# Kernel optimization log

Measured on AMD Instinct MI355X. Metric: run time of the kernel, lower is better.

Reference implementation:

```python
import jax, jax.numpy as jnp
import numpy as np

TOKEN_SIZE = 4
NEIGHBOR_SIZE = 3


def setup_inputs() -> dict:
    key = jax.random.key(0)
    ks = jax.random.split(key, 8)
    B, C, H, W = 8, 256, 64, 64
    return {
        "blue_feat": jax.random.normal(ks[0], (B, C, H, W), jnp.float32),
        "white_feat": jax.random.normal(ks[1], (B, C, H, W), jnp.float32),
        "Wq": jax.random.normal(ks[2], (C, C), jnp.float32) * 0.05,
        "bq": jax.random.normal(ks[3], (C,), jnp.float32) * 0.05,
        "Wk": jax.random.normal(ks[4], (C, C), jnp.float32) * 0.05,
        "bk": jax.random.normal(ks[5], (C,), jnp.float32) * 0.05,
        "Wv": jax.random.normal(ks[6], (C, C), jnp.float32) * 0.05,
        "bv": jax.random.normal(ks[7], (C,), jnp.float32) * 0.05,
    }


def _tokens(x, nh, nw, ts):
    # [B,C,H,W] -> [B,nh,nw,C,ts*ts]
    B, C = x.shape[0], x.shape[1]
    return (x.reshape(B, C, nh, ts, nw, ts)
             .transpose(0, 2, 4, 1, 3, 5)
             .reshape(B, nh, nw, C, ts * ts))


def reference(blue_feat, white_feat, Wq, bq, Wk, bk, Wv, bv):
    ts, ns = TOKEN_SIZE, NEIGHBOR_SIZE
    pad = ns // 2
    B, C, H, W = blue_feat.shape
    scale = float((ts * ts) ** -0.5)

    # 1x1 conv projections (pointwise channel mix + bias)
    Q = jnp.einsum('bchw,oc->bohw', blue_feat, Wq) + bq[None, :, None, None]
    K = jnp.einsum('bchw,oc->bohw', white_feat, Wk) + bk[None, :, None, None]
    V = jnp.einsum('bchw,oc->bohw', white_feat, Wv) + bv[None, :, None, None]

    nh, nw = H // ts, W // ts  # H,W divisible by ts -> no padding branch
    Qt = _tokens(Q, nh, nw, ts)  # [B,nh,nw,C,D]
    Kt = _tokens(K, nh, nw, ts)
    Vt = _tokens(V, nh, nw, ts)

    # zero-padded token grid, gather 3x3 neighbor tokens (F.unfold equivalent)
    padw = ((0, 0), (pad, pad), (pad, pad), (0, 0), (0, 0))
    Kp = jnp.pad(Kt, padw)
    Vp = jnp.pad(Vt, padw)
    Knb = jnp.stack([Kp[:, di:di + nh, dj:dj + nw]
                     for di in range(ns) for dj in range(ns)], axis=3)  # [B,nh,nw,9,C,D]
    Vnb = jnp.stack([Vp[:, di:di + nh, dj:dj + nw]
                     for di in range(ns) for dj in range(ns)], axis=3)

    # per-channel attention over neighbor tokens
    attn = jax.nn.softmax(
        jnp.einsum('bhwcd,bhwncd->bhwcn', Qt, Knb) * scale, axis=-1)
    out = jnp.einsum('bhwcn,bhwncd->bhwcd', attn, Vnb)  # [B,nh,nw,C,D]

    enhanced = (out.reshape(B, nh, nw, C, ts, ts)
                   .transpose(0, 3, 1, 4, 2, 5)
                   .reshape(B, C, H, W))
    return blue_feat + enhanced  # out_proj is Identity since c1 == c2
```

## Files before the change

### kernel.cpp

```cpp
#include <hip/hip_runtime.h>
#include <hip/hip_bf16.h>
#include <stdint.h>

typedef float  f32x4  __attribute__((ext_vector_type(4)));
typedef float  f32x2  __attribute__((ext_vector_type(2)));
typedef __bf16 bf16x8 __attribute__((ext_vector_type(8)));

#define LROW 40

__global__ __launch_bounds__(1024) void prep_kernel(
    const float* __restrict__ blue, const float* __restrict__ white,
    const float* __restrict__ Wq, const float* __restrict__ Wk,
    const float* __restrict__ Wv,
    __bf16* __restrict__ Xtb, __bf16* __restrict__ Xtw,
    __bf16* __restrict__ Wbf)
{
  const int bid = blockIdx.x;
  const int tid = threadIdx.x;

  if (bid >= 256) {
    const int t = bid - 256;
    const float* src = (t == 0) ? Wq : (t == 1) ? Wk : Wv;
    __bf16* dst = Wbf + t * 65536;
#pragma unroll
    for (int it = 0; it < 8; ++it) {
      const int idx = it * 8192 + tid * 8;
      f32x4 v0 = *(const f32x4*)(src + idx);
      f32x4 v1 = *(const f32x4*)(src + idx + 4);
      bf16x8 r;
#pragma unroll
      for (int q = 0; q < 4; ++q) { r[q] = (__bf16)v0[q]; r[q + 4] = (__bf16)v1[q]; }
      *(bf16x8*)(dst + idx) = r;
    }
    return;
  }

  const int srcw = bid >> 7;
  const int rem  = bid & 127;
  const int b    = rem >> 4;
  const int ti   = rem & 15;
  const float* X = srcw ? white : blue;
  __bf16*     Xt = srcw ? Xtw : Xtb;

  const int s  = tid & 7;
  const int co = (tid >> 3) & 31;
  const int u  = tid >> 8;

  const float* Xb = X + (size_t)b * (256 * 4096);
  __bf16* Xtb2 = Xt + (size_t)b * 4096 * 256;

#pragma unroll
  for (int it = 0; it < 4; ++it) {
    const int p   = u * 32 + it * 8 + s;
    const int px  = 2 * p;
    const int r   = px >> 6;
    const int col = px & 63;
    const int hw  = (ti * 4 + r) * 64 + col;
    const int d   = r * 4 + (col & 3);
    const int n   = ti * 256 + (col >> 2) * 16 + d;

    bf16x8 e0, e1;
#pragma unroll
    for (int j = 0; j < 8; ++j) {
      const int c = co * 8 + j;
      f32x2 v = *(const f32x2*)(Xb + (size_t)c * 4096 + hw);
      e0[j] = (__bf16)v[0];
      e1[j] = (__bf16)v[1];
    }
    *(bf16x8*)(Xtb2 + (size_t)n * 256 + co * 8)       = e0;
    *(bf16x8*)(Xtb2 + (size_t)(n + 1) * 256 + co * 8) = e1;
  }
}


#define GLOAD16(GS, LD) \
  __builtin_amdgcn_global_load_lds( \
      (const __attribute__((address_space(1))) uint32_t*)(GS), \
      (__attribute__((address_space(3))) uint32_t*)(LD), 16, 0, 0)

__global__ __launch_bounds__(256) void gemm_lds_kernel(
    const __bf16* __restrict__ Xtb, const __bf16* __restrict__ Xtw,
    const __bf16* __restrict__ Wbf,
    const float* __restrict__ bq, const float* __restrict__ bk,
    const float* __restrict__ bv,
    __bf16* __restrict__ Qt, __bf16* __restrict__ Kt, __bf16* __restrict__ Vt)
{
  __shared__ __bf16 As[2][128 * 32];
  __shared__ __bf16 Bs[2][128 * 32];

  const int bid = blockIdx.x;
  const int lid = (bid & 7) * 192 + (bid >> 3);
  const int nb  = lid / 6;
  const int bt  = lid % 6;
  const int tensor = (bt < 4) ? 1 + (bt & 1) : 0;
  const int ob     = (bt < 4) ? (bt >> 1) : (bt & 1);

  const __bf16* Xt   = (tensor == 0) ? Xtb : Xtw;
  const float*  bias = (tensor == 0) ? bq : (tensor == 1) ? bk : bv;
  __bf16*       Out  = (tensor == 0) ? Qt : (tensor == 1) ? Kt : Vt;
  const __bf16* Wp   = Wbf + tensor * 65536 + ob * 32768;

  const int tid  = threadIdx.x;
  const int lane = tid & 63;
  const int w    = tid >> 6;
  const int wo   = w >> 1;
  const int wn   = w & 1;
  const int lrow = lane & 15;
  const int lks  = lane >> 4;

  const int o0 = ob * 128;
  const int n0 = nb * 128;

  const int l     = lane;
  const int rA    = w * 16 + (l >> 2);
  const int gslot = (l & 3) ^ ((l >> 3) & 3);
  const __bf16* gA = Wp + (size_t)rA * 256 + gslot * 8;
  const __bf16* gB = Xt + (size_t)(n0 + rA) * 256 + gslot * 8;
  const int ldsOffQ0 = (w * 16) * 32;
  const int ldsOffQ1 = (64 + w * 16) * 32;

#define STAGE(BUF, KK) do {                                        \
    GLOAD16(gA + (KK) * 32,             &As[BUF][ldsOffQ0]);       \
    GLOAD16(gA + 64 * 256 + (KK) * 32,  &As[BUF][ldsOffQ1]);       \
    GLOAD16(gB + (KK) * 32,             &Bs[BUF][ldsOffQ0]);       \
    GLOAD16(gB + 64 * 256 + (KK) * 32,  &Bs[BUF][ldsOffQ1]);       \
  } while (0)

  const int sx = ((lks ^ ((lrow >> 1) & 3)) * 8);

  f32x4 acc[4][4];
#pragma unroll
  for (int i = 0; i < 4; ++i)
#pragma unroll
    for (int j = 0; j < 4; ++j) acc[i][j] = (f32x4)0.0f;

#define COMPUTE(BUF) do {                                                       \
    bf16x8 af[4], bfr[4];                                                       \
    _Pragma("unroll")                                                           \
    for (int i = 0; i < 4; ++i)                                                 \
      af[i] = *(const bf16x8*)&As[BUF][(wo * 64 + i * 16 + lrow) * 32 + sx];    \
    _Pragma("unroll")                                                           \
    for (int j = 0; j < 4; ++j)                                                 \
      bfr[j] = *(const bf16x8*)&Bs[BUF][(wn * 64 + j * 16 + lrow) * 32 + sx];   \
    _Pragma("unroll")                                                           \
    for (int i = 0; i < 4; ++i)                                                 \
      _Pragma("unroll")                                                         \
      for (int j = 0; j < 4; ++j)                                               \
        acc[i][j] = __builtin_amdgcn_mfma_f32_16x16x32_bf16(af[i], bfr[j],      \
                                                            acc[i][j], 0, 0, 0);\
  } while (0)

  STAGE(0, 0);
  __syncthreads();
#pragma unroll
  for (int kp = 0; kp < 4; ++kp) {
    STAGE(1, 2 * kp + 1);
    COMPUTE(0);
    __syncthreads();
    if (kp < 3) STAGE(0, 2 * kp + 2);
    COMPUTE(1);
    __syncthreads();
  }
#undef STAGE
#undef COMPUTE

#pragma unroll
  for (int i = 0; i < 4; ++i) {
    const int obase = o0 + wo * 64 + i * 16 + (lane >> 4) * 4;
#pragma unroll
    for (int j = 0; j < 4; ++j) {
      const int n  = n0 + wn * 64 + j * 16 + (lane & 15);
      const int bb = n >> 12;
      const int pp = n & 4095;
      const int tt = pp >> 4;
      const int tii = tt >> 4;
      const int tjj = tt & 15;
      const int dd  = pp & 15;
      const size_t base = ((size_t)(bb * 16 + tii) * 256) * 256 + tjj * 16 + dd;
#pragma unroll
      for (int r = 0; r < 4; ++r) {
        const int o = obase + r;
        const float v = acc[i][j][r] + bias[o];
        Out[base + (size_t)o * 256] = (__bf16)v;
      }
    }
  }
}

__global__ __launch_bounds__(256) void proj_gemm_kernel(
    const float* __restrict__ blue, const float* __restrict__ white,
    const float* __restrict__ Wq, const float* __restrict__ bq,
    const float* __restrict__ Wk, const float* __restrict__ bk,
    const float* __restrict__ Wv, const float* __restrict__ bv,
    __bf16* __restrict__ Qt, __bf16* __restrict__ Kt, __bf16* __restrict__ Vt)
{
  __shared__ __bf16 As[128 * LROW];
  __shared__ __bf16 Bs[128 * LROW];

  const int bidhw = blockIdx.x;
  const int lid   = (bidhw & 7) * 192 + (bidhw >> 3);
  const int nb    = lid / 6;
  const int bt    = lid % 6;
  const int tensor = (bt < 4) ? 1 + (bt & 1) : 0;
  const int ob     = (bt < 4) ? (bt >> 1) : (bt & 1);

  const float* X    = (tensor == 0) ? blue : white;
  const float* W    = (tensor == 0) ? Wq : (tensor == 1) ? Wk : Wv;
  const float* bias = (tensor == 0) ? bq : (tensor == 1) ? bk : bv;
  __bf16*      Out  = (tensor == 0) ? Qt : (tensor == 1) ? Kt : Vt;

  const int tid  = threadIdx.x;
  const int lane = tid & 63;
  const int wave = tid >> 6;
  const int wo   = wave >> 1;
  const int wn   = wave & 1;

  const int o0 = ob * 128;
  const int n0 = nb * 128;
  const int batch = n0 >> 12;
  const int p0    = n0 & 4095;
  const int tk0   = p0 >> 4;
  const int trow  = tk0 >> 4;
  const int tcol0 = tk0 & 15;
  const float* Xb = X + (size_t)batch * (256 * 4096);

  f32x4 acc[4][4];
#pragma unroll
  for (int i = 0; i < 4; ++i)
#pragma unroll
    for (int j = 0; j < 4; ++j) acc[i][j] = (f32x4)0.0f;

  const int arow  = tid >> 1;
  const int ahalf = tid & 1;
  const int n2   = tid & 63;
  const int ko   = tid >> 6;
  const int nloc = 2 * n2;
  const int tl   = nloc >> 4;
  const int d    = nloc & 15;
  const int hw   = (trow * 4 + (d >> 2)) * 64 + (tcol0 + tl) * 4 + (d & 3);

  const int lrow = lane & 15;
  const int lk   = (lane >> 4) * 8;

  for (int kk = 0; kk < 8; ++kk) {
    const int k0 = kk * 32;
    {
      const float* src = W + (size_t)(o0 + arow) * 256 + k0 + ahalf * 16;
      f32x4 t0 = *(const f32x4*)(src + 0);
      f32x4 t1 = *(const f32x4*)(src + 4);
      f32x4 t2 = *(const f32x4*)(src + 8);
      f32x4 t3 = *(const f32x4*)(src + 12);
      bf16x8 c0, c1;
#pragma unroll
      for (int qq = 0; qq < 4; ++qq) { c0[qq] = (__bf16)t0[qq]; c0[qq + 4] = (__bf16)t1[qq]; }
#pragma unroll
      for (int qq = 0; qq < 4; ++qq) { c1[qq] = (__bf16)t2[qq]; c1[qq + 4] = (__bf16)t3[qq]; }
      __bf16* dst = As + arow * LROW + ahalf * 16;
      *(bf16x8*)(dst + 0) = c0;
      *(bf16x8*)(dst + 8) = c1;
    }
    {
      const float* src = Xb + (size_t)(k0 + ko * 8) * 4096 + hw;
      f32x2 v0 = *(const f32x2*)(src + 0 * 4096);
      f32x2 v1 = *(const f32x2*)(src + 1 * 4096);
      f32x2 v2 = *(const f32x2*)(src + 2 * 4096);
      f32x2 v3 = *(const f32x2*)(src + 3 * 4096);
      f32x2 v4 = *(const f32x2*)(src + 4 * 4096);
      f32x2 v5 = *(const f32x2*)(src + 5 * 4096);
      f32x2 v6 = *(const f32x2*)(src + 6 * 4096);
      f32x2 v7 = *(const f32x2*)(src + 7 * 4096);
      bf16x8 r0, r1;
      r0[0] = (__bf16)v0[0]; r0[1] = (__bf16)v1[0]; r0[2] = (__bf16)v2[0]; r0[3] = (__bf16)v3[0];
      r0[4] = (__bf16)v4[0]; r0[5] = (__bf16)v5[0]; r0[6] = (__bf16)v6[0]; r0[7] = (__bf16)v7[0];
      r1[0] = (__bf16)v0[1]; r1[1] = (__bf16)v1[1]; r1[2] = (__bf16)v2[1]; r1[3] = (__bf16)v3[1];
      r1[4] = (__bf16)v4[1]; r1[5] = (__bf16)v5[1]; r1[6] = (__bf16)v6[1]; r1[7] = (__bf16)v7[1];
      *(bf16x8*)(Bs + (nloc + 0) * LROW + ko * 8) = r0;
      *(bf16x8*)(Bs + (nloc + 1) * LROW + ko * 8) = r1;
    }
    __syncthreads();

    bf16x8 a[4], b[4];
#pragma unroll
    for (int i = 0; i < 4; ++i)
      a[i] = *(const bf16x8*)(As + (wo * 64 + i * 16 + lrow) * LROW + lk);
#pragma unroll
    for (int j = 0; j < 4; ++j)
      b[j] = *(const bf16x8*)(Bs + (wn * 64 + j * 16 + lrow) * LROW + lk);
#pragma unroll
    for (int i = 0; i < 4; ++i)
#pragma unroll
      for (int j = 0; j < 4; ++j)
        acc[i][j] = __builtin_amdgcn_mfma_f32_16x16x32_bf16(a[i], b[j], acc[i][j], 0, 0, 0);
    __syncthreads();
  }

#pragma unroll
  for (int i = 0; i < 4; ++i) {
    const int obase = o0 + wo * 64 + i * 16 + (lane >> 4) * 4;
#pragma unroll
    for (int j = 0; j < 4; ++j) {
      const int n  = n0 + wn * 64 + j * 16 + (lane & 15);
      const int bb = n >> 12;
      const int p  = n & 4095;
      const int tt = p >> 4;
      const int tii = tt >> 4;
      const int tjj = tt & 15;
      const int dd  = p & 15;
      const size_t base = ((size_t)(bb * 16 + tii) * 256) * 256 + tjj * 16 + dd;
#pragma unroll
      for (int r = 0; r < 4; ++r) {
        const int o = obase + r;
        const float v = acc[i][j][r] + bias[o];
        Out[base + (size_t)o * 256] = (__bf16)v;
      }
    }
  }
}

__device__ __forceinline__ void unpack8(const uint4 v, float* f) {
  const uint32_t u0 = v.x, u1 = v.y, u2 = v.z, u3 = v.w;
  f[0] = __uint_as_float(u0 << 16); f[1] = __uint_as_float(u0 & 0xffff0000u);
  f[2] = __uint_as_float(u1 << 16); f[3] = __uint_as_float(u1 & 0xffff0000u);
  f[4] = __uint_as_float(u2 << 16); f[5] = __uint_as_float(u2 & 0xffff0000u);
  f[6] = __uint_as_float(u3 << 16); f[7] = __uint_as_float(u3 & 0xffff0000u);
}

__global__ __launch_bounds__(256) void attn_kernel(
    const __bf16* __restrict__ Qt, const __bf16* __restrict__ Kt,
    const __bf16* __restrict__ Vt, const float* __restrict__ blue,
    float* __restrict__ out)
{
  const int j   = blockIdx.x;
  const int bid = (j & 7) * 256 + (j >> 3);
  const int cg  = bid & 15;
  const int ti  = (bid >> 4) & 15;
  const int b   = bid >> 8;

  const int tid = threadIdx.x;
  const int tj  = tid & 15;
  const int cl  = tid >> 4;
  const int c   = cg * 16 + cl;

  float q[16];
  {
    const __bf16* p = Qt + ((((size_t)b * 16 + ti) * 256 + c) * 16 + tj) * 16;
    unpack8(*(const uint4*)p, q);
    unpack8(*(const uint4*)(p + 8), q + 8);
  }

  float s[9];
#pragma unroll
  for (int n = 0; n < 9; ++n) {
    const int yi = ti + n / 3 - 1;
    const int yj = tj + n % 3 - 1;
    float dot = 0.0f;
    if (yi >= 0 && yi < 16 && yj >= 0 && yj < 16) {
      const __bf16* p = Kt + ((((size_t)b * 16 + yi) * 256 + c) * 16 + yj) * 16;
      float kf[16];
      unpack8(*(const uint4*)p, kf);
      unpack8(*(const uint4*)(p + 8), kf + 8);
#pragma unroll
      for (int dd = 0; dd < 16; ++dd) dot = fmaf(q[dd], kf[dd], dot);
    }
    s[n] = dot * 0.25f;
  }

  float m = s[0];
#pragma unroll
  for (int n = 1; n < 9; ++n) m = fmaxf(m, s[n]);
  float w[9], denom = 0.0f;
#pragma unroll
  for (int n = 0; n < 9; ++n) { w[n] = __expf(s[n] - m); denom += w[n]; }
  const float inv = 1.0f / denom;

  float o16[16];
#pragma unroll
  for (int dd = 0; dd < 16; ++dd) o16[dd] = 0.0f;
#pragma unroll
  for (int n = 0; n < 9; ++n) {
    const int yi = ti + n / 3 - 1;
    const int yj = tj + n % 3 - 1;
    if (yi >= 0 && yi < 16 && yj >= 0 && yj < 16) {
      const __bf16* p = Vt + ((((size_t)b * 16 + yi) * 256 + c) * 16 + yj) * 16;
      float vf[16];
      unpack8(*(const uint4*)p, vf);
      unpack8(*(const uint4*)(p + 8), vf + 8);
#pragma unroll
      for (int dd = 0; dd < 16; ++dd) o16[dd] = fmaf(w[n], vf[dd], o16[dd]);
    }
  }

  const size_t pbase = ((size_t)b * 256 + c) * 4096 + (size_t)(ti * 4) * 64 + tj * 4;
#pragma unroll
  for (int r = 0; r < 4; ++r) {
    f32x4 bl = *(const f32x4*)(blue + pbase + r * 64);
    f32x4 ov;
#pragma unroll
    for (int j2 = 0; j2 < 4; ++j2) ov[j2] = bl[j2] + o16[r * 4 + j2] * inv;
    *(f32x4*)(out + pbase + r * 64) = ov;
  }
}

extern "C" void kernel_launch(void* const* d_in, const int* in_sizes, int n_in,
                              void* d_out, int out_size, void* d_ws, size_t ws_size,
                              hipStream_t stream) {
  const float* blue  = (const float*)d_in[0];
  const float* white = (const float*)d_in[1];
  const float* Wq = (const float*)d_in[2];
  const float* bq = (const float*)d_in[3];
  const float* Wk = (const float*)d_in[4];
  const float* bk = (const float*)d_in[5];
  const float* Wv = (const float*)d_in[6];
  const float* bv = (const float*)d_in[7];
  float* out = (float*)d_out;

  const size_t tsz = (size_t)8 * 256 * 256 * 16;
  const size_t xsz = (size_t)8 * 4096 * 256;
  __bf16* Qt = (__bf16*)d_ws;
  __bf16* Kt = Qt + tsz;
  __bf16* Vt = Kt + tsz;

  const size_t need_new = (3 * tsz + 2 * xsz + 3 * 65536) * sizeof(__bf16);
  if (ws_size >= need_new) {
    __bf16* Xtb = Vt + tsz;
    __bf16* Xtw = Xtb + xsz;
    __bf16* Wbf = Xtw + xsz;
    prep_kernel<<<259, 1024, 0, stream>>>(blue, white, Wq, Wk, Wv, Xtb, Xtw, Wbf);
    gemm_lds_kernel<<<1536, 256, 0, stream>>>(Xtb, Xtw, Wbf, bq, bk, bv, Qt, Kt, Vt);
  } else {
    proj_gemm_kernel<<<1536, 256, 0, stream>>>(blue, white, Wq, bq, Wk, bk, Wv, bv, Qt, Kt, Vt);
  }
  attn_kernel<<<2048, 256, 0, stream>>>(Qt, Kt, Vt, blue, out);
}
```

Measured before the change: 72.65 us.

## Triple-buffer GEMM LDS staging with explicit vmcnt waits and MFMA priority

Switches the projection GEMM from double to triple buffering of A/B tiles in LDS. Two loads stay in flight while the current tile is computed, using explicit s_waitcnt vmcnt counts and raw s_barrier calls in place of __syncthreads. It also raises wave priority around the MFMA block. The aim is to hide global-to-LDS load latency better, at the cost of 50% more LDS per block, which may lower occupancy. The hand-tuned vmcnt counts are also fragile.

```diff
diff --git a/kernel.cpp b/kernel.cpp
--- a/kernel.cpp
+++ b/kernel.cpp
@@ -85,8 +85,8 @@
     const float* __restrict__ bv,
     __bf16* __restrict__ Qt, __bf16* __restrict__ Kt, __bf16* __restrict__ Vt)
 {
-  __shared__ __bf16 As[2][128 * 32];
-  __shared__ __bf16 Bs[2][128 * 32];
+  __shared__ __bf16 As[3][128 * 32];
+  __shared__ __bf16 Bs[3][128 * 32];
 
   const int bid = blockIdx.x;
   const int lid = (bid & 7) * 192 + (bid >> 3);
@@ -142,25 +142,39 @@
     _Pragma("unroll")                                                           \
     for (int j = 0; j < 4; ++j)                                                 \
       bfr[j] = *(const bf16x8*)&Bs[BUF][(wn * 64 + j * 16 + lrow) * 32 + sx];   \
+    __builtin_amdgcn_s_setprio(1);                                              \
     _Pragma("unroll")                                                           \
     for (int i = 0; i < 4; ++i)                                                 \
       _Pragma("unroll")                                                         \
       for (int j = 0; j < 4; ++j)                                               \
         acc[i][j] = __builtin_amdgcn_mfma_f32_16x16x32_bf16(af[i], bfr[j],      \
                                                             acc[i][j], 0, 0, 0);\
+    __builtin_amdgcn_s_setprio(0);                                              \
   } while (0)
 
   STAGE(0, 0);
-  __syncthreads();
-#pragma unroll
-  for (int kp = 0; kp < 4; ++kp) {
-    STAGE(1, 2 * kp + 1);
-    COMPUTE(0);
-    __syncthreads();
-    if (kp < 3) STAGE(0, 2 * kp + 2);
-    COMPUTE(1);
-    __syncthreads();
-  }
+  STAGE(1, 1);
+  STAGE(2, 2);
+
+#define PHASE(T) do {                                                           \
+    if ((T) >= 6) {                                                             \
+      if ((T) == 6) asm volatile("s_waitcnt vmcnt(4)" ::: "memory");            \
+      else          asm volatile("s_waitcnt vmcnt(0)" ::: "memory");            \
+    } else          asm volatile("s_waitcnt vmcnt(8)" ::: "memory");            \
+    __builtin_amdgcn_sched_barrier(0);                                          \
+    __builtin_amdgcn_s_barrier();                                               \
+    __builtin_amdgcn_sched_barrier(0);                                          \
+    COMPUTE((T) % 3);                                                           \
+    asm volatile("s_waitcnt lgkmcnt(0)" ::: "memory");                          \
+    __builtin_amdgcn_sched_barrier(0);                                          \
+    __builtin_amdgcn_s_barrier();                                               \
+    __builtin_amdgcn_sched_barrier(0);                                          \
+    if ((T) < 5) STAGE((T) % 3, (T) + 3);                                       \
+  } while (0)
+
+  PHASE(0); PHASE(1); PHASE(2); PHASE(3);
+  PHASE(4); PHASE(5); PHASE(6); PHASE(7);
+#undef PHASE
 #undef STAGE
 #undef COMPUTE
 
```

Result: faster. 70.76 us (-2.6%).
